# Kernel tuning notes

Hardware: AMD Instinct MI355X
Metric: run time of the kernel (lower is better)

Reference implementation:

```python
import jax, jax.numpy as jnp
import numpy as np

N = 30000      # entities
E = 200000     # KG triples
E_ALL = 400000 # full-graph edges
R = 500        # relations
EH = 300       # e_hidden
RH = 100       # r_hidden
H = 8          # GAT / R2E heads
H_E2R = 2      # E2R heads: int(softmax(head_selector).sum()+1) == 2 always
EPS = 1e-16    # torch_geometric softmax eps


def _seg_softmax(logits, idx, num):
    # logits: [E, heads]; segment-wise stable softmax over edges grouped by idx
    m = jax.ops.segment_max(logits, idx, num_segments=num)
    ex = jnp.exp(logits - m[idx])
    s = jax.ops.segment_sum(ex, idx, num_segments=num)
    return ex / (s[idx] + EPS)


def _gcn(x, ei):
    j, i = ei[0], ei[1]
    deg = jax.ops.segment_sum(jnp.ones(ei.shape[1], x.dtype), i, num_segments=N)
    dis = jnp.where(deg > 0, deg ** -0.5, 0.0)
    norm = dis[j] * dis[i]                                        # [E_all]
    agg = jax.ops.segment_sum(norm[:, None] * x[j], i, num_segments=N)
    return jax.nn.relu(agg)


def _highway(x1, x2, w, b):
    gate = jax.nn.sigmoid(x1 @ w.T + b)
    return gate * x2 + (1.0 - gate) * x1


def setup_inputs() -> dict:
    key = jax.random.key(0)
    ks = jax.random.split(key, 20)
    f = jnp.float32
    inp = {
        'x_e': jax.random.normal(ks[0], (N, EH), f),
        'edge_index': jax.random.randint(ks[1], (2, E), 0, N),
        'rel': jax.random.randint(ks[2], (E,), 0, R),
        'edge_index_all': jax.random.randint(ks[3], (2, E_ALL), 0, N),
        'rel_all': jax.random.randint(ks[4], (E_ALL,), 0, R),
        # Highway layers
        'hw1_w': jax.random.normal(ks[5], (EH, EH), f) / np.sqrt(EH),
        'hw1_b': jnp.zeros((EH,), f),
        'hw2_w': jax.random.normal(ks[6], (EH, EH), f) / np.sqrt(EH),
        'hw2_b': jnp.zeros((EH,), f),
        # E2R (only first H_E2R heads are ever used)
        'e2r_wh': jax.random.normal(ks[7], (RH, EH), f) / np.sqrt(EH),
        'e2r_wt': jax.random.normal(ks[8], (RH, EH), f) / np.sqrt(EH),
        'e2r_ah': jax.random.normal(ks[9], (H_E2R, RH), f) / np.sqrt(RH),
        'e2r_at': jax.random.normal(ks[10], (H_E2R, RH), f) / np.sqrt(RH),
        # R2E
        'r2e_ah': jax.random.normal(ks[11], (H, EH), f) / np.sqrt(EH),
        'r2e_at': jax.random.normal(ks[12], (H, EH), f) / np.sqrt(EH),
        'r2e_ar': jax.random.normal(ks[13], (H, RH), f) / np.sqrt(RH),
        # GAT over e_hidden + 2*r_hidden = 500
        'gat_ai': jax.random.normal(ks[14], (H, EH + 2 * RH), f) / np.sqrt(EH + 2 * RH),
        'gat_aj': jax.random.normal(ks[15], (H, EH + 2 * RH), f) / np.sqrt(EH + 2 * RH),
    }
    return inp


def reference(x_e, edge_index, rel, edge_index_all, rel_all,
              hw1_w, hw1_b, hw2_w, hw2_b,
              e2r_wh, e2r_wt, e2r_ah, e2r_at,
              r2e_ah, r2e_at, r2e_ar, gat_ai, gat_aj):
    lrelu = jax.nn.leaky_relu  # slope 0.01, matches torch default

    # --- two GCN + Highway blocks (dropout = identity at eval) ---
    x = _highway(x_e, _gcn(x_e, edge_index_all), hw1_w, hw1_b)
    x = _highway(x, _gcn(x, edge_index_all), hw2_w, hw2_b)

    h_idx, t_idx = edge_index[0], edge_index[1]

    # --- E2R: entity -> relation (2 heads; spmm sum over heads folded into alpha sum) ---
    xh = x @ e2r_wh.T                        # [N, RH]
    xt = x @ e2r_wt.T                        # [N, RH]
    e1 = (xh @ e2r_ah.T)[h_idx] + (xt @ e2r_at.T)[t_idx]   # [E, H_E2R]
    a1 = _seg_softmax(lrelu(e1), rel, R)
    xr_h = jax.ops.segment_sum(a1.sum(1)[:, None] * xh[h_idx], rel, num_segments=R)
    e2 = (xt @ e2r_ah.T)[h_idx] + (xh @ e2r_at.T)[t_idx]
    a2 = _seg_softmax(lrelu(e2), rel, R)
    xr_t = jax.ops.segment_sum(a2.sum(1)[:, None] * xt[t_idx], rel, num_segments=R)
    x_r = (xr_h + xr_t) / H_E2R / 2.0        # [R, RH]

    # --- R2E: relation -> entity (8 heads) ---
    se_h = x @ r2e_ah.T                      # [N, H]
    se_t = x @ r2e_at.T
    sr = x_r @ r2e_ar.T                      # [R, H]
    a_h = _seg_softmax(lrelu(se_h[h_idx] + sr[rel]), h_idx, N)
    a_t = _seg_softmax(lrelu(se_t[t_idx] + sr[rel]), t_idx, N)
    xr_rel = x_r[rel]                        # [E, RH]
    xe_h = jax.ops.segment_sum(a_h.sum(1)[:, None] * xr_rel, h_idx, num_segments=N) / H
    xe_t = jax.ops.segment_sum(a_t.sum(1)[:, None] * xr_rel, t_idx, num_segments=N) / H
    x2 = jnp.concatenate([x, xe_h, xe_t], axis=1)          # [N, EH+2*RH]

    # --- GAT over full graph (8 heads) ---
    j_a, i_a = edge_index_all[0], edge_index_all[1]
    e_ij = (x2 @ gat_ai.T)[i_a] + (x2 @ gat_aj.T)[j_a]     # [E_all, H]
    al = _seg_softmax(lrelu(e_ij), i_a, N)
    x_gat = jax.ops.segment_sum(al.sum(1)[:, None] * x2[j_a], i_a, num_segments=N) / H

    return jnp.concatenate([x2, x_gat], axis=1)            # [N, 2*(EH+2*RH)]
```

## Files before the change

### kernel.cpp

```cpp
#include <hip/hip_runtime.h>
#include <math.h>

constexpr int N_    = 30000;
constexpr int E_    = 200000;
constexpr int EALL_ = 400000;
constexpr int R_    = 500;
constexpr int EH_   = 300;
constexpr int RH_   = 100;
constexpr int OUTD_ = 1000;
constexpr int LD4   = OUTD_/4;
constexpr int EH4   = EH_/4;
constexpr int RH4   = RH_/4;
constexpr int NC_   = 16;
constexpr int XBS_  = 320;
constexpr int XEBS_ = 200;
constexpr int KP_   = 320;
constexpr int NBR_  = 64;
constexpr int PERB_ = (E_ + NBR_ - 1)/NBR_;
constexpr int SCB_  = 2048;
constexpr int NSB_  = (N_ + SCB_ - 1)/SCB_;
constexpr int SCNP_ = NSB_*SCB_;

typedef __attribute__((ext_vector_type(4))) float f32x4;
typedef __attribute__((ext_vector_type(8))) short s16x8;

__device__ __forceinline__ float lrelu_(float v){ return v > 0.f ? v : 0.01f*v; }
__device__ __forceinline__ float sig_(float z){ return 1.f/(1.f + expf(-z)); }
__device__ __forceinline__ unsigned short f2bf_(float f){
  unsigned int u = __float_as_uint(f);
  unsigned int r = (u + 0x7FFFu + ((u >> 16) & 1u)) >> 16;
  return (unsigned short)r;
}
__device__ __forceinline__ float bf2f_(unsigned short h){
  return __uint_as_float(((unsigned int)h) << 16);
}

__global__ void k_count3(const int* __restrict__ ia,
                         const int* __restrict__ hi, const int* __restrict__ ti,
                         int* cd, int* ch, int* ct){
  int idx = blockIdx.x*blockDim.x + threadIdx.x;
  if (idx < EALL_) { atomicAdd(&cd[ia[idx]], 1); return; }
  idx -= EALL_;
  if (idx < E_) { atomicAdd(&ch[hi[idx]], 1); return; }
  idx -= E_;
  if (idx < E_) { atomicAdd(&ct[ti[idx]], 1); return; }
}

__global__ void k_scanA(const int* __restrict__ c0, const int* __restrict__ c1,
                        const int* __restrict__ c2, int* __restrict__ bsum){
  int arr = blockIdx.x / NSB_, b = blockIdx.x - arr*NSB_;
  const int* c = arr == 0 ? c0 : (arr == 1 ? c1 : c2);
  int t = threadIdx.x;
  const int4* c4 = reinterpret_cast<const int4*>(c + b*SCB_ + t*8);
  int4 u0 = c4[0], u1 = c4[1];
  int acc = u0.x+u0.y+u0.z+u0.w + u1.x+u1.y+u1.z+u1.w;
  __shared__ int red[256];
  red[t] = acc;
  __syncthreads();
  for (int o = 128; o > 0; o >>= 1){
    if (t < o) red[t] += red[t+o];
    __syncthreads();
  }
  if (t == 0) bsum[arr*NSB_ + b] = red[0];
}

__global__ void k_scanB(int* __restrict__ bsum, int* o0, int* o1, int* o2){
  int t = threadIdx.x;
  if (t < 3){
    int run = 0;
    for (int b = 0; b < NSB_; ++b){ int v = bsum[t*NSB_ + b]; bsum[t*NSB_ + b] = run; run += v; }
    int* o = t == 0 ? o0 : (t == 1 ? o1 : o2);
    o[N_] = run;
  }
}

__global__ void k_scanC(const int* __restrict__ c0, const int* __restrict__ c1,
                        const int* __restrict__ c2, const int* __restrict__ bsum,
                        int* o0, int* o1, int* o2, float* __restrict__ dis){
  int arr = blockIdx.x / NSB_, b = blockIdx.x - arr*NSB_;
  const int* c = arr == 0 ? c0 : (arr == 1 ? c1 : c2);
  int* o = arr == 0 ? o0 : (arr == 1 ? o1 : o2);
  int t = threadIdx.x;
  int base = b*SCB_ + t*8;
  const int4* c4 = reinterpret_cast<const int4*>(c + base);
  int4 u0 = c4[0], u1 = c4[1];
  int v[8] = {u0.x,u0.y,u0.z,u0.w,u1.x,u1.y,u1.z,u1.w};
  int tot = v[0]+v[1]+v[2]+v[3]+v[4]+v[5]+v[6]+v[7];
  __shared__ int sc[256];
  sc[t] = tot;
  __syncthreads();
  for (int off = 1; off < 256; off <<= 1){
    int add = (t >= off) ? sc[t-off] : 0;
    __syncthreads();
    sc[t] += add;
    __syncthreads();
  }
  int run = bsum[arr*NSB_ + b] + (t ? sc[t-1] : 0);
  #pragma unroll
  for (int i = 0; i < 8; ++i){
    int idx = base + i;
    o[idx] = run;
    if (arr == 0) dis[idx] = v[i] > 0 ? rsqrtf((float)v[i]) : 0.f;
    run += v[i];
  }
}

__global__ void k_scatter3(const int* __restrict__ ja, const int* __restrict__ ia,
                           const int* __restrict__ rel, const int* __restrict__ hi,
                           const int* __restrict__ ti,
                           const int* od, const int* oh, const int* ot,
                           int* curd, int* curh, int* curt,
                           const float* __restrict__ dis,
                           int* j_dest, float* wj,
                           int* relh, int* relt){
  int idx = blockIdx.x*blockDim.x + threadIdx.x;
  if (idx < EALL_){
    int e = idx, s = ia[e];
    int p = od[s] + atomicAdd(&curd[s], 1);
    int j = ja[e];
    j_dest[p] = j; wj[p] = dis[j]; return;
  }
  idx -= EALL_;
  if (idx < E_){
    int e = idx, s = hi[e];
    int p = oh[s] + atomicAdd(&curh[s], 1);
    relh[p] = rel[e]; return;
  }
  idx -= E_;
  if (idx < E_){
    int e = idx, s = ti[e];
    int p = ot[s] + atomicAdd(&curt[s], 1);
    relt[p] = rel[e]; return;
  }
}

__global__ void k_relhist(const int* __restrict__ rel, int* __restrict__ H){
  __shared__ int h[R_];
  int b = blockIdx.x, tid = threadIdx.x;
  for (int i = tid; i < R_; i += 256) h[i] = 0;
  __syncthreads();
  int s = b*PERB_, e = min(s + PERB_, E_);
  for (int i = s + tid; i < e; i += 256) atomicAdd(&h[rel[i]], 1);
  __syncthreads();
  for (int i = tid; i < R_; i += 256) H[b*R_ + i] = h[i];
}

__global__ void k_relscan(int* __restrict__ H, int* __restrict__ off_rel){
  __shared__ int tot[R_];
  __shared__ int sc[256];
  int tid = threadIdx.x;
  for (int r = tid; r < R_; r += 256){
    int acc = 0;
    for (int b = 0; b < NBR_; ++b){ int v = H[b*R_ + r]; H[b*R_ + r] = acc; acc += v; }
    tot[r] = acc;
  }
  __syncthreads();
  int r0 = tid*2;
  int a0 = (r0 < R_) ? tot[r0] : 0;
  int a1 = (r0+1 < R_) ? tot[r0+1] : 0;
  sc[tid] = a0 + a1;
  __syncthreads();
  for (int off = 1; off < 256; off <<= 1){
    int add = (tid >= off) ? sc[tid-off] : 0;
    __syncthreads();
    sc[tid] += add;
    __syncthreads();
  }
  int run = tid ? sc[tid-1] : 0;
  if (r0 < R_)   off_rel[r0]   = run;
  if (r0+1 < R_) off_rel[r0+1] = run + a0;
  if (tid == 255) off_rel[R_] = sc[255];
  __syncthreads();
  for (int r = tid; r < R_; r += 256){
    int o = off_rel[r];
    for (int b = 0; b < NBR_; ++b) H[b*R_ + r] += o;
  }
}

__global__ void k_relscatter(const int* __restrict__ rel, const int* __restrict__ hi,
                             const int* __restrict__ ti, const int* __restrict__ H,
                             int* __restrict__ hr, int* __restrict__ tr){
  __shared__ int cur[R_];
  int b = blockIdx.x, tid = threadIdx.x;
  for (int i = tid; i < R_; i += 256) cur[i] = H[b*R_ + i];
  __syncthreads();
  int s = b*PERB_, e = min(s + PERB_, E_);
  for (int i = s + tid; i < e; i += 256){
    int r = rel[i];
    int p = atomicAdd(&cur[r], 1);
    hr[p] = hi[i]; tr[p] = ti[i];
  }
}

__global__ void k_pack_x(const float4* __restrict__ X, int ldx4,
                         unsigned short* __restrict__ xb){
  int idx = blockIdx.x*blockDim.x + threadIdx.x;
  if (idx >= N_*80) return;
  int n = idx / 80, c = idx - n*80;
  ushort4 o = make_ushort4(0,0,0,0);
  if (c < EH4){
    float4 v = X[(size_t)n*ldx4 + c];
    o.x = f2bf_(v.x); o.y = f2bf_(v.y); o.z = f2bf_(v.z); o.w = f2bf_(v.w);
  }
  *reinterpret_cast<ushort4*>(&xb[(size_t)n*XBS_ + c*4]) = o;
}

__global__ void k_pack_weights(const float* __restrict__ w1, const float* __restrict__ w2,
                               const float* __restrict__ wh, const float* __restrict__ wt,
                               unsigned short* w1b, unsigned short* w2b,
                               unsigned short* wcb){
  int idx = blockIdx.x*blockDim.x + threadIdx.x;
  if (idx < EH_*KP_){
    int n = idx/KP_, k = idx - n*KP_;
    w1b[idx] = (k < EH_) ? f2bf_(w1[(size_t)n*EH_ + k]) : (unsigned short)0;
    return;
  }
  idx -= EH_*KP_;
  if (idx < EH_*KP_){
    int n = idx/KP_, k = idx - n*KP_;
    w2b[idx] = (k < EH_) ? f2bf_(w2[(size_t)n*EH_ + k]) : (unsigned short)0;
    return;
  }
  idx -= EH_*KP_;
  if (idx < 200*KP_){
    int n = idx/KP_, k = idx - n*KP_;
    wcb[idx] = (k < EH_) ? f2bf_((n < 100) ? wh[(size_t)n*EH_ + k] : wt[(size_t)(n-100)*EH_ + k])
                         : (unsigned short)0;
  }
}

__global__ __launch_bounds__(256) void k_gemm_mfma(
    const unsigned short* __restrict__ Ab,
    const unsigned short* __restrict__ Wb,
    float* __restrict__ C, int ldc, int M, int Nn){
  constexpr int WS = 328;
  constexpr int AS = 40;
  __shared__ unsigned short Ws[64*WS];
  __shared__ unsigned short As[128*AS];
  int tid = threadIdx.x;
  int lane = tid & 63, wave = tid >> 6;
  int wm = wave & 1, wn = wave >> 1;
  int m0 = blockIdx.x*128, n0 = blockIdx.y*64;

  for (int c = tid; c < 64*(KP_/8); c += 256){
    int n = c / (KP_/8), k8 = (c % (KP_/8))*8;
    s16x8 v = {0,0,0,0,0,0,0,0};
    if (n0 + n < Nn)
      v = *reinterpret_cast<const s16x8*>(&Wb[(size_t)(n0+n)*KP_ + k8]);
    *reinterpret_cast<s16x8*>(&Ws[n*WS + k8]) = v;
  }

  f32x4 acc[4][2] = {};
  int kf = (lane >> 4)*8;
  int rA = lane & 15;
  for (int k0 = 0; k0 < KP_; k0 += 32){
    __syncthreads();
    for (int c = tid; c < 128*4; c += 256){
      int r = c >> 2, k8 = (c & 3)*8;
      s16x8 v = {0,0,0,0,0,0,0,0};
      if (m0 + r < M)
        v = *reinterpret_cast<const s16x8*>(&Ab[(size_t)(m0+r)*XBS_ + k0 + k8]);
      *reinterpret_cast<s16x8*>(&As[r*AS + k8]) = v;
    }
    __syncthreads();
    s16x8 afr[4], bfr[2];
    #pragma unroll
    for (int mf = 0; mf < 4; ++mf)
      afr[mf] = *reinterpret_cast<const s16x8*>(&As[(wm*64 + mf*16 + rA)*AS + kf]);
    #pragma unroll
    for (int nf = 0; nf < 2; ++nf)
      bfr[nf] = *reinterpret_cast<const s16x8*>(&Ws[(wn*32 + nf*16 + rA)*WS + k0 + kf]);
    #pragma unroll
    for (int mf = 0; mf < 4; ++mf)
      #pragma unroll
      for (int nf = 0; nf < 2; ++nf)
        acc[mf][nf] = __builtin_amdgcn_mfma_f32_16x16x32_bf16(afr[mf], bfr[nf], acc[mf][nf], 0, 0, 0);
  }
  int col0 = n0 + wn*32 + (lane & 15);
  int rbase = m0 + wm*64 + (lane >> 4)*4;
  #pragma unroll
  for (int mf = 0; mf < 4; ++mf){
    #pragma unroll
    for (int nf = 0; nf < 2; ++nf){
      int col = col0 + nf*16;
      if (col < Nn){
        #pragma unroll
        for (int r = 0; r < 4; ++r){
          int row = rbase + mf*16 + r;
          if (row < M) C[(size_t)row*ldc + col] = acc[mf][nf][r];
        }
      }
    }
  }
}

__global__ void k_gcn5(const int* __restrict__ off, const int* __restrict__ jd,
                       const float* __restrict__ wj, const float* __restrict__ dis,
                       const unsigned short* __restrict__ xsrc,
                       const float4* __restrict__ Xold, int ldo4,
                       const float4* __restrict__ G, const float* __restrict__ b,
                       float4* __restrict__ Xn, unsigned short* __restrict__ xdst){
  __shared__ int js[64];
  __shared__ float ws[64];
  int n = blockIdx.x, lane = threadIdx.x;
  int s = off[n], t = off[n+1];
  bool two = lane < (EH4 - 64);
  float4 a0 = make_float4(0.f,0.f,0.f,0.f);
  float4 a1 = make_float4(0.f,0.f,0.f,0.f);
  for (int base = s; base < t; base += 64){
    int m = min(64, t - base);
    __syncthreads();
    if (lane < m){ js[lane] = jd[base+lane]; ws[lane] = wj[base+lane]; }
    __syncthreads();
    int q = 0;
    for (; q + 3 < m; q += 4){
      size_t r0 = (size_t)js[q]*XBS_,   r1 = (size_t)js[q+1]*XBS_;
      size_t r2 = (size_t)js[q+2]*XBS_, r3 = (size_t)js[q+3]*XBS_;
      float w0 = ws[q], w1 = ws[q+1], w2 = ws[q+2], w3 = ws[q+3];
      ushort4 u0 = *reinterpret_cast<const ushort4*>(&xsrc[r0 + lane*4]);
      ushort4 u1 = *reinterpret_cast<const ushort4*>(&xsrc[r1 + lane*4]);
      ushort4 u2 = *reinterpret_cast<const ushort4*>(&xsrc[r2 + lane*4]);
      ushort4 u3 = *reinterpret_cast<const ushort4*>(&xsrc[r3 + lane*4]);
      a0.x += w0*bf2f_(u0.x)+w1*bf2f_(u1.x)+w2*bf2f_(u2.x)+w3*bf2f_(u3.x);
      a0.y += w0*bf2f_(u0.y)+w1*bf2f_(u1.y)+w2*bf2f_(u2.y)+w3*bf2f_(u3.y);
      a0.z += w0*bf2f_(u0.z)+w1*bf2f_(u1.z)+w2*bf2f_(u2.z)+w3*bf2f_(u3.z);
      a0.w += w0*bf2f_(u0.w)+w1*bf2f_(u1.w)+w2*bf2f_(u2.w)+w3*bf2f_(u3.w);
      if (two){
        ushort4 v0 = *reinterpret_cast<const ushort4*>(&xsrc[r0 + 256 + lane*4]);
        ushort4 v1 = *reinterpret_cast<const ushort4*>(&xsrc[r1 + 256 + lane*4]);
        ushort4 v2 = *reinterpret_cast<const ushort4*>(&xsrc[r2 + 256 + lane*4]);
        ushort4 v3 = *reinterpret_cast<const ushort4*>(&xsrc[r3 + 256 + lane*4]);
        a1.x += w0*bf2f_(v0.x)+w1*bf2f_(v1.x)+w2*bf2f_(v2.x)+w3*bf2f_(v3.x);
        a1.y += w0*bf2f_(v0.y)+w1*bf2f_(v1.y)+w2*bf2f_(v2.y)+w3*bf2f_(v3.y);
        a1.z += w0*bf2f_(v0.z)+w1*bf2f_(v1.z)+w2*bf2f_(v2.z)+w3*bf2f_(v3.z);
        a1.w += w0*bf2f_(v0.w)+w1*bf2f_(v1.w)+w2*bf2f_(v2.w)+w3*bf2f_(v3.w);
      }
    }
    for (; q < m; ++q){
      size_t r0 = (size_t)js[q]*XBS_;
      float w0 = ws[q];
      ushort4 u0 = *reinterpret_cast<const ushort4*>(&xsrc[r0 + lane*4]);
      a0.x += w0*bf2f_(u0.x); a0.y += w0*bf2f_(u0.y);
      a0.z += w0*bf2f_(u0.z); a0.w += w0*bf2f_(u0.w);
      if (two){
        ushort4 v0 = *reinterpret_cast<const ushort4*>(&xsrc[r0 + 256 + lane*4]);
        a1.x += w0*bf2f_(v0.x); a1.y += w0*bf2f_(v0.y);
        a1.z += w0*bf2f_(v0.z); a1.w += w0*bf2f_(v0.w);
      }
    }
  }
  float dn = dis[n];
  {
    int c = lane;
    float4 yv;
    yv.x = fmaxf(dn*a0.x, 0.f); yv.y = fmaxf(dn*a0.y, 0.f);
    yv.z = fmaxf(dn*a0.z, 0.f); yv.w = fmaxf(dn*a0.w, 0.f);
    float4 g4 = G[(size_t)n*EH4 + c];
    float4 b4 = reinterpret_cast<const float4*>(b)[c];
    float4 xo = Xold[(size_t)n*ldo4 + c];
    float gx; float4 r;
    gx = sig_(g4.x + b4.x); r.x = gx*yv.x + (1.f-gx)*xo.x;
    gx = sig_(g4.y + b4.y); r.y = gx*yv.y + (1.f-gx)*xo.y;
    gx = sig_(g4.z + b4.z); r.z = gx*yv.z + (1.f-gx)*xo.z;
    gx = sig_(g4.w + b4.w); r.w = gx*yv.w + (1.f-gx)*xo.w;
    Xn[(size_t)n*LD4 + c] = r;
    ushort4 o;
    o.x = f2bf_(r.x); o.y = f2bf_(r.y); o.z = f2bf_(r.z); o.w = f2bf_(r.w);
    *reinterpret_cast<ushort4*>(&xdst[(size_t)n*XBS_ + c*4]) = o;
  }
  if (two){
    int c = 64 + lane;
    float4 yv;
    yv.x = fmaxf(dn*a1.x, 0.f); yv.y = fmaxf(dn*a1.y, 0.f);
    yv.z = fmaxf(dn*a1.z, 0.f); yv.w = fmaxf(dn*a1.w, 0.f);
    float4 g4 = G[(size_t)n*EH4 + c];
    float4 b4 = reinterpret_cast<const float4*>(b)[c];
    float4 xo = Xold[(size_t)n*ldo4 + c];
    float gx; float4 r;
    gx = sig_(g4.x + b4.x); r.x = gx*yv.x + (1.f-gx)*xo.x;
    gx = sig_(g4.y + b4.y); r.y = gx*yv.y + (1.f-gx)*xo.y;
    gx = sig_(g4.z + b4.z); r.z = gx*yv.z + (1.f-gx)*xo.z;
    gx = sig_(g4.w + b4.w); r.w = gx*yv.w + (1.f-gx)*xo.w;
    Xn[(size_t)n*LD4 + c] = r;
    ushort4 o;
    o.x = f2bf_(r.x); o.y = f2bf_(r.y); o.z = f2bf_(r.z); o.w = f2bf_(r.w);
    *reinterpret_cast<ushort4*>(&xdst[(size_t)n*XBS_ + c*4]) = o;
  } else if (lane < 16){
    ushort4 z = make_ushort4(0,0,0,0);
    *reinterpret_cast<ushort4*>(&xdst[(size_t)n*XBS_ + (64+lane)*4]) = z;
  }
}

__global__ void k_pproj(const float* __restrict__ xhxt,
                        const float* __restrict__ ah, const float* __restrict__ at,
                        float4* __restrict__ pht){
  int n = blockIdx.x*blockDim.x + threadIdx.x;
  if (n >= N_) return;
  float a0=0,a1=0,b0=0,b1=0,c0=0,c1=0,d0=0,d1=0;
  const float* xh = xhxt + (size_t)n*200;
  const float* xt = xh + 100;
  for (int f = 0; f < RH_; ++f) {
    float vh = xh[f], vt = xt[f];
    float w0 = ah[f], w1 = ah[RH_+f], u0 = at[f], u1 = at[RH_+f];
    a0 += vh*w0; a1 += vh*w1;
    b0 += vt*u0; b1 += vt*u1;
    c0 += vt*w0; c1 += vt*w1;
    d0 += vh*u0; d1 += vh*u1;
  }
  pht[(size_t)n*2]     = make_float4(a0, a1, c0, c1);
  pht[(size_t)n*2 + 1] = make_float4(b0, b1, d0, d1);
}

__global__ void k_fold_rel2(const int* __restrict__ off,
                            const int* __restrict__ hr, const int* __restrict__ tr,
                            const float4* __restrict__ pht,
                            float* __restrict__ s1p, float* __restrict__ s2p){
  __shared__ float4 redm[4];
  __shared__ float4 reds[4];
  int r = blockIdx.x;
  int tid = threadIdx.x, lane = tid & 63, w = tid >> 6;
  int s = off[r], e = off[r+1];
  float4 mx = make_float4(-1e30f,-1e30f,-1e30f,-1e30f);
  for (int p = s + tid; p < e; p += 256){
    float4 ph = pht[(size_t)hr[p]*2];
    float4 pt = pht[(size_t)tr[p]*2 + 1];
    mx.x = fmaxf(mx.x, lrelu_(ph.x + pt.x));
    mx.y = fmaxf(mx.y, lrelu_(ph.y + pt.y));
    mx.z = fmaxf(mx.z, lrelu_(ph.z + pt.z));
    mx.w = fmaxf(mx.w, lrelu_(ph.w + pt.w));
  }
  #pragma unroll
  for (int o = 1; o < 64; o <<= 1){
    mx.x = fmaxf(mx.x, __shfl_xor(mx.x, o));
    mx.y = fmaxf(mx.y, __shfl_xor(mx.y, o));
    mx.z = fmaxf(mx.z, __shfl_xor(mx.z, o));
    mx.w = fmaxf(mx.w, __shfl_xor(mx.w, o));
  }
  if (lane == 0) redm[w] = mx;
  __syncthreads();
  float4 m;
  m.x = fmaxf(fmaxf(redm[0].x, redm[1].x), fmaxf(redm[2].x, redm[3].x));
  m.y = fmaxf(fmaxf(redm[0].y, redm[1].y), fmaxf(redm[2].y, redm[3].y));
  m.z = fmaxf(fmaxf(redm[0].z, redm[1].z), fmaxf(redm[2].z, redm[3].z));
  m.w = fmaxf(fmaxf(redm[0].w, redm[1].w), fmaxf(redm[2].w, redm[3].w));
  float4 sm = make_float4(0.f,0.f,0.f,0.f);
  for (int p = s + tid; p < e; p += 256){
    float4 ph = pht[(size_t)hr[p]*2];
    float4 pt = pht[(size_t)tr[p]*2 + 1];
    sm.x += expf(lrelu_(ph.x + pt.x) - m.x);
    sm.y += expf(lrelu_(ph.y + pt.y) - m.y);
    sm.z += expf(lrelu_(ph.z + pt.z) - m.z);
    sm.w += expf(lrelu_(ph.w + pt.w) - m.w);
  }
  #pragma unroll
  for (int o = 1; o < 64; o <<= 1){
    sm.x += __shfl_xor(sm.x, o);
    sm.y += __shfl_xor(sm.y, o);
    sm.z += __shfl_xor(sm.z, o);
    sm.w += __shfl_xor(sm.w, o);
  }
  if (lane == 0) reds[w] = sm;
  __syncthreads();
  float4 sv;
  sv.x = reds[0].x + reds[1].x + reds[2].x + reds[3].x;
  sv.y = reds[0].y + reds[1].y + reds[2].y + reds[3].y;
  sv.z = reds[0].z + reds[1].z + reds[2].z + reds[3].z;
  sv.w = reds[0].w + reds[1].w + reds[2].w + reds[3].w;
  float4 inv;
  inv.x = 1.f/(sv.x + 1e-16f); inv.y = 1.f/(sv.y + 1e-16f);
  inv.z = 1.f/(sv.z + 1e-16f); inv.w = 1.f/(sv.w + 1e-16f);
  for (int p = s + tid; p < e; p += 256){
    float4 ph = pht[(size_t)hr[p]*2];
    float4 pt = pht[(size_t)tr[p]*2 + 1];
    s1p[p] = expf(lrelu_(ph.x + pt.x) - m.x)*inv.x + expf(lrelu_(ph.y + pt.y) - m.y)*inv.y;
    s2p[p] = expf(lrelu_(ph.z + pt.z) - m.z)*inv.z + expf(lrelu_(ph.w + pt.w) - m.w)*inv.w;
  }
}

__global__ void k_fold_ht2(const int* __restrict__ offh, const int* __restrict__ offt,
                           const int* __restrict__ relh, const int* __restrict__ relt,
                           const float* __restrict__ st16, const float* __restrict__ sr8,
                           float* __restrict__ shp, float* __restrict__ stp){
  int w = threadIdx.x >> 6, lane = threadIdx.x & 63;
  int n = blockIdx.x*2 + (w >> 1);
  if (n >= N_) return;
  int side = w & 1;
  const int* off = side ? offt : offh;
  const int* rl  = side ? relt : relh;
  float* op = side ? stp : shp;
  int k = lane & 7, g = lane >> 3;
  float cst = st16[(size_t)n*16 + side*8 + k];
  int s = off[n], e = off[n+1];
  float m = -1e30f;
  for (int p = s + g; p < e; p += 8)
    m = fmaxf(m, lrelu_(cst + sr8[(size_t)rl[p]*8 + k]));
  #pragma unroll
  for (int o = 8; o < 64; o <<= 1) m = fmaxf(m, __shfl_xor(m, o));
  float sum = 0.f;
  for (int p = s + g; p < e; p += 8)
    sum += expf(lrelu_(cst + sr8[(size_t)rl[p]*8 + k]) - m);
  #pragma unroll
  for (int o = 8; o < 64; o <<= 1) sum += __shfl_xor(sum, o);
  float inv = 1.f / (sum + 1e-16f);
  for (int p = s + g; p < e; p += 8){
    float t = expf(lrelu_(cst + sr8[(size_t)rl[p]*8 + k]) - m) * inv;
    #pragma unroll
    for (int o = 1; o < 8; o <<= 1) t += __shfl_xor(t, o);
    if (k == 0) op[p] = t;
  }
}

__global__ void k_fold_gat2(const int* __restrict__ off, const int* __restrict__ jd,
                            const float* __restrict__ gg16, float* __restrict__ agp){
  int w = threadIdx.x >> 6, lane = threadIdx.x & 63;
  int n = blockIdx.x*4 + w;
  if (n >= N_) return;
  int k = lane & 7, g = lane >> 3;
  float cst = gg16[(size_t)n*16 + k];
  int s = off[n], e = off[n+1];
  float m = -1e30f;
  for (int p = s + g; p < e; p += 8)
    m = fmaxf(m, lrelu_(cst + gg16[(size_t)jd[p]*16 + 8 + k]));
  #pragma unroll
  for (int o = 8; o < 64; o <<= 1) m = fmaxf(m, __shfl_xor(m, o));
  float sum = 0.f;
  for (int p = s + g; p < e; p += 8)
    sum += expf(lrelu_(cst + gg16[(size_t)jd[p]*16 + 8 + k]) - m);
  #pragma unroll
  for (int o = 8; o < 64; o <<= 1) sum += __shfl_xor(sum, o);
  float inv = 1.f / (sum + 1e-16f);
  for (int p = s + g; p < e; p += 8){
    float t = expf(lrelu_(cst + gg16[(size_t)jd[p]*16 + 8 + k]) - m) * inv;
    #pragma unroll
    for (int o = 1; o < 8; o <<= 1) t += __shfl_xor(t, o);
    if (k == 0) agp[p] = t;
  }
}

__global__ void k_e2r_agg3(const int* __restrict__ off,
                           const int* __restrict__ hr, const int* __restrict__ tr,
                           const float* __restrict__ s1p, const float* __restrict__ s2p,
                           const float4* __restrict__ xhxt4, float4* __restrict__ xr_part){
  int r = blockIdx.x, c = blockIdx.y;
  int lane = threadIdx.x;
  int side = lane >> 5, fl = lane & 31;
  int s = off[r], e = off[r+1];
  int len = e - s;
  int per = (len + NC_ - 1)/NC_;
  int cs = s + c*per, ce = min(cs + per, e);
  float4 acc = make_float4(0.f,0.f,0.f,0.f);
  if (fl < RH4){
    const int* idx = side ? tr : hr;
    const float* wv = side ? s2p : s1p;
    int fofs = side ? 25 + fl : fl;
    int p = cs;
    for (; p + 1 < ce; p += 2){
      float a0 = wv[p], a1 = wv[p+1];
      float4 v0 = xhxt4[(size_t)idx[p]*50 + fofs];
      float4 v1 = xhxt4[(size_t)idx[p+1]*50 + fofs];
      acc.x += a0*v0.x + a1*v1.x; acc.y += a0*v0.y + a1*v1.y;
      acc.z += a0*v0.z + a1*v1.z; acc.w += a0*v0.w + a1*v1.w;
    }
    if (p < ce){
      float a0 = wv[p];
      float4 v0 = xhxt4[(size_t)idx[p]*50 + fofs];
      acc.x += a0*v0.x; acc.y += a0*v0.y; acc.z += a0*v0.z; acc.w += a0*v0.w;
    }
  }
  float4 oth;
  oth.x = __shfl_xor(acc.x, 32); oth.y = __shfl_xor(acc.y, 32);
  oth.z = __shfl_xor(acc.z, 32); oth.w = __shfl_xor(acc.w, 32);
  if (side == 0 && fl < RH4){
    float4 o = make_float4(acc.x+oth.x, acc.y+oth.y, acc.z+oth.z, acc.w+oth.w);
    xr_part[((size_t)c*R_ + r)*RH4 + fl] = o;
  }
}

__global__ void k_e2r_red2(const float4* __restrict__ xr_part, float4* __restrict__ xr4,
                           const float* __restrict__ ar, float* __restrict__ sr8){
  __shared__ float row[RH_];
  int r = blockIdx.x, lane = threadIdx.x;
  if (lane < RH4){
    float4 a = make_float4(0.f,0.f,0.f,0.f);
    #pragma unroll
    for (int c = 0; c < NC_; ++c){
      float4 v = xr_part[((size_t)c*R_ + r)*RH4 + lane];
      a.x += v.x; a.y += v.y; a.z += v.z; a.w += v.w;
    }
    a.x *= 0.25f; a.y *= 0.25f; a.z *= 0.25f; a.w *= 0.25f;
    xr4[(size_t)r*RH4 + lane] = a;
    row[lane*4]   = a.x; row[lane*4+1] = a.y;
    row[lane*4+2] = a.z; row[lane*4+3] = a.w;
  }
  __syncthreads();
  int h = lane & 7, gk = lane >> 3;
  float acc = 0.f;
  for (int k = gk; k < RH_; k += 8) acc += row[k]*ar[(size_t)h*RH_ + k];
  #pragma unroll
  for (int o = 8; o < 64; o <<= 1) acc += __shfl_xor(acc, o);
  if (lane < 8) sr8[(size_t)r*8 + lane] = acc;
}

__global__ void k_dots16b(const unsigned short* __restrict__ X, int ldx, int K, int colofs, int Kw,
                          const float* __restrict__ wA, const float* __restrict__ wB,
                          float* __restrict__ out16, int M, int accum){
  __shared__ float xs[16][65];
  __shared__ float ws[16][65];
  int tid = threadIdx.x;
  int tx = tid & 15, ty = tid >> 4;
  int r0 = blockIdx.x*16;
  int lr = tid >> 4;
  int lc = (tid & 15)*4;
  float acc = 0.f;
  for (int c0 = 0; c0 < K; c0 += 64){
    int cl = min(64, K - c0);
    float4 xv = make_float4(0.f,0.f,0.f,0.f);
    if (r0 + lr < M && lc < cl){
      ushort4 u = *reinterpret_cast<const ushort4*>(&X[(size_t)(r0+lr)*ldx + c0 + lc]);
      xv.x = bf2f_(u.x); xv.y = bf2f_(u.y); xv.z = bf2f_(u.z); xv.w = bf2f_(u.w);
    }
    float4 wv = make_float4(0.f,0.f,0.f,0.f);
    if (lc < cl){
      const float* wsrc = (lr < 8) ? &wA[(size_t)lr*Kw + colofs + c0 + lc]
                                   : &wB[(size_t)(lr-8)*Kw + colofs + c0 + lc];
      wv = *reinterpret_cast<const float4*>(wsrc);
    }
    xs[lr][lc] = xv.x; xs[lr][lc+1] = xv.y; xs[lr][lc+2] = xv.z; xs[lr][lc+3] = xv.w;
    ws[lr][lc] = wv.x; ws[lr][lc+1] = wv.y; ws[lr][lc+2] = wv.z; ws[lr][lc+3] = wv.w;
    __syncthreads();
    #pragma unroll
    for (int k = 0; k < 64; ++k) acc += xs[ty][k]*ws[tx][k];
    __syncthreads();
  }
  if (r0 + ty < M){
    size_t o = (size_t)(r0+ty)*16 + tx;
    out16[o] = accum ? out16[o] + acc : acc;
  }
}

__global__ void k_r2e_agg2b(const int* __restrict__ offh, const int* __restrict__ offt,
                            const int* __restrict__ relh, const int* __restrict__ relt,
                            const float* __restrict__ shp, const float* __restrict__ stp,
                            const float4* __restrict__ xr4, float4* __restrict__ out,
                            unsigned short* __restrict__ xeb){
  int n = blockIdx.x;
  int side = threadIdx.x >> 6, lane = threadIdx.x & 63;
  const int* off = side ? offt : offh;
  const int* rr  = side ? relt : relh;
  const float* sp = side ? stp : shp;
  int s = off[n], e = off[n+1];
  if (lane >= RH4) return;
  float4 acc = make_float4(0.f,0.f,0.f,0.f);
  int p = s;
  for (; p + 1 < e; p += 2){
    float a0 = sp[p], a1 = sp[p+1];
    float4 v0 = xr4[(size_t)rr[p]*RH4 + lane];
    float4 v1 = xr4[(size_t)rr[p+1]*RH4 + lane];
    acc.x += a0*v0.x + a1*v1.x; acc.y += a0*v0.y + a1*v1.y;
    acc.z += a0*v0.z + a1*v1.z; acc.w += a0*v0.w + a1*v1.w;
  }
  if (p < e){
    float a0 = sp[p];
    float4 v0 = xr4[(size_t)rr[p]*RH4 + lane];
    acc.x += a0*v0.x; acc.y += a0*v0.y; acc.z += a0*v0.z; acc.w += a0*v0.w;
  }
  float4 o = make_float4(acc.x*0.125f, acc.y*0.125f, acc.z*0.125f, acc.w*0.125f);
  out[(size_t)n*LD4 + (side ? 100 : 75) + lane] = o;
  ushort4 ob;
  ob.x = f2bf_(o.x); ob.y = f2bf_(o.y); ob.z = f2bf_(o.z); ob.w = f2bf_(o.w);
  *reinterpret_cast<ushort4*>(&xeb[(size_t)n*XEBS_ + (side ? 100 : 0) + lane*4]) = ob;
}

__global__ void k_gat_agg4(const int* __restrict__ off, const int* __restrict__ jd,
                           const float* __restrict__ agp,
                           const unsigned short* __restrict__ xb,
                           const unsigned short* __restrict__ xeb,
                           float4* __restrict__ out){
  __shared__ int js[128];
  __shared__ float as_[128];
  int n = blockIdx.x, tid = threadIdx.x;
  int s = off[n], t = off[n+1];
  const unsigned short* tbl;
  size_t stride; int cofs;
  if (tid < 75){ tbl = xb;  stride = XBS_;  cofs = tid*4; }
  else         { tbl = xeb; stride = XEBS_; cofs = (tid-75)*4; }
  float4 acc = make_float4(0.f,0.f,0.f,0.f);
  for (int base = s; base < t; base += 128){
    int m = min(128, t - base);
    __syncthreads();
    if (tid < m){ js[tid] = jd[base+tid]; as_[tid] = agp[base+tid]; }
    __syncthreads();
    if (tid < 125){
      int q = 0;
      for (; q + 3 < m; q += 4){
        float a0 = as_[q], a1 = as_[q+1], a2 = as_[q+2], a3 = as_[q+3];
        ushort4 u0 = *reinterpret_cast<const ushort4*>(&tbl[(size_t)js[q]*stride + cofs]);
        ushort4 u1 = *reinterpret_cast<const ushort4*>(&tbl[(size_t)js[q+1]*stride + cofs]);
        ushort4 u2 = *reinterpret_cast<const ushort4*>(&tbl[(size_t)js[q+2]*stride + cofs]);
        ushort4 u3 = *reinterpret_cast<const ushort4*>(&tbl[(size_t)js[q+3]*stride + cofs]);
        acc.x += a0*bf2f_(u0.x)+a1*bf2f_(u1.x)+a2*bf2f_(u2.x)+a3*bf2f_(u3.x);
        acc.y += a0*bf2f_(u0.y)+a1*bf2f_(u1.y)+a2*bf2f_(u2.y)+a3*bf2f_(u3.y);
        acc.z += a0*bf2f_(u0.z)+a1*bf2f_(u1.z)+a2*bf2f_(u2.z)+a3*bf2f_(u3.z);
        acc.w += a0*bf2f_(u0.w)+a1*bf2f_(u1.w)+a2*bf2f_(u2.w)+a3*bf2f_(u3.w);
      }
      for (; q < m; ++q){
        float a0 = as_[q];
        ushort4 u0 = *reinterpret_cast<const ushort4*>(&tbl[(size_t)js[q]*stride + cofs]);
        acc.x += a0*bf2f_(u0.x); acc.y += a0*bf2f_(u0.y);
        acc.z += a0*bf2f_(u0.z); acc.w += a0*bf2f_(u0.w);
      }
    }
  }
  if (tid < 125){
    float4 r = make_float4(acc.x*0.125f, acc.y*0.125f, acc.z*0.125f, acc.w*0.125f);
    out[(size_t)n*LD4 + 125 + tid] = r;
  }
}

static inline void gemm_mfma(const unsigned short* Ab, const unsigned short* Wb,
                             float* C, int ldc, int M, int Nn, hipStream_t st){
  dim3 g((M + 127)/128, (Nn + 63)/64);
  k_gemm_mfma<<<g, 256, 0, st>>>(Ab, Wb, C, ldc, M, Nn);
}

extern "C" void kernel_launch(void* const* d_in, const int* in_sizes, int n_in,
                              void* d_out, int out_size, void* d_ws, size_t ws_size,
                              hipStream_t stream) {
  const float* x_e   = (const float*)d_in[0];
  const int*   ei    = (const int*)d_in[1];
  const int*   rel   = (const int*)d_in[2];
  const int*   eia   = (const int*)d_in[3];
  const float* hw1_w = (const float*)d_in[5];
  const float* hw1_b = (const float*)d_in[6];
  const float* hw2_w = (const float*)d_in[7];
  const float* hw2_b = (const float*)d_in[8];
  const float* e2r_wh= (const float*)d_in[9];
  const float* e2r_wt= (const float*)d_in[10];
  const float* e2r_ah= (const float*)d_in[11];
  const float* e2r_at= (const float*)d_in[12];
  const float* r2e_ah= (const float*)d_in[13];
  const float* r2e_at= (const float*)d_in[14];
  const float* r2e_ar= (const float*)d_in[15];
  const float* gat_ai= (const float*)d_in[16];
  const float* gat_aj= (const float*)d_in[17];
  float* out = (float*)d_out;

  const int* hi = ei;
  const int* ti = ei + E_;
  const int* ja = eia;
  const int* ia = eia + EALL_;

  char* base = (char*)d_ws;
  size_t off = 0;
  auto alloc = [&](size_t bytes)->void*{
    void* p = base + off;
    off = (off + bytes + 255) & ~(size_t)255;
    return p;
  };

  size_t z0 = off;
  int* cnt_dest = (int*)alloc(SCNP_*4);
  int* cnt_h    = (int*)alloc(SCNP_*4);
  int* cnt_t    = (int*)alloc(SCNP_*4);
  int* cur_dest = (int*)alloc(N_*4);
  int* cur_h    = (int*)alloc(N_*4);
  int* cur_t    = (int*)alloc(N_*4);
  size_t z1 = off;

  int* off_dest = (int*)alloc(SCNP_*4);
  int* off_h    = (int*)alloc(SCNP_*4);
  int* off_t    = (int*)alloc(SCNP_*4);
  int* off_rel  = (int*)alloc((R_+1)*4);
  int* bsum     = (int*)alloc(3*NSB_*4);
  int* Hrel     = (int*)alloc((size_t)NBR_*R_*4);
  int* j_dest   = (int*)alloc((size_t)EALL_*4);
  int* hr       = (int*)alloc((size_t)E_*4);
  int* tr       = (int*)alloc((size_t)E_*4);
  int* relh     = (int*)alloc((size_t)E_*4);
  int* relt     = (int*)alloc((size_t)E_*4);

  float* dis   = (float*)alloc(SCNP_*4);
  float* wj    = (float*)alloc((size_t)EALL_*4);
  float* g     = (float*)alloc((size_t)N_*EH_*4);
  float* xhxt  = (float*)alloc((size_t)N_*200*4);
  float* pht   = (float*)alloc((size_t)N_*8*4);
  float* s1p   = (float*)alloc((size_t)E_*4);
  float* s2p   = (float*)alloc((size_t)E_*4);
  float* xr    = (float*)alloc((size_t)R_*RH_*4);
  float* xr_part=(float*)alloc((size_t)NC_*R_*RH_*4);
  float* st16  = (float*)alloc((size_t)N_*16*4);
  float* sr8   = (float*)alloc((size_t)R_*8*4);
  float* shp   = (float*)alloc((size_t)E_*4);
  float* stp   = (float*)alloc((size_t)E_*4);
  float* gg16  = (float*)alloc((size_t)N_*16*4);
  float* agp   = (float*)alloc((size_t)EALL_*4);
  unsigned short* xbA = (unsigned short*)alloc((size_t)N_*XBS_*2);
  unsigned short* xbB = (unsigned short*)alloc((size_t)N_*XBS_*2);
  unsigned short* xeb = (unsigned short*)alloc((size_t)N_*XEBS_*2);
  unsigned short* w1b = (unsigned short*)alloc((size_t)EH_*KP_*2);
  unsigned short* w2b = (unsigned short*)alloc((size_t)EH_*KP_*2);
  unsigned short* wcb = (unsigned short*)alloc((size_t)200*KP_*2);

  hipMemsetAsync(base + z0, 0, z1 - z0, stream);

  const int TB = 256;
  const int TOT = EALL_ + 2*E_;
  int gTOT  = (TOT + TB - 1)/TB;
  int gN    = (N_ + TB - 1)/TB;
  int gPKX  = (N_*80 + TB - 1)/TB;
  const int WTOT = 2*EH_*KP_ + 200*KP_;

  k_pack_weights<<<(WTOT + TB - 1)/TB, TB, 0, stream>>>(hw1_w, hw2_w, e2r_wh, e2r_wt,
                                                        w1b, w2b, wcb);

  k_relhist<<<NBR_, 256, 0, stream>>>(rel, Hrel);
  k_relscan<<<1, 256, 0, stream>>>(Hrel, off_rel);
  k_relscatter<<<NBR_, 256, 0, stream>>>(rel, hi, ti, Hrel, hr, tr);

  k_count3<<<gTOT, TB, 0, stream>>>(ia, hi, ti, cnt_dest, cnt_h, cnt_t);
  k_scanA<<<3*NSB_, 256, 0, stream>>>(cnt_dest, cnt_h, cnt_t, bsum);
  k_scanB<<<1, 64, 0, stream>>>(bsum, off_dest, off_h, off_t);
  k_scanC<<<3*NSB_, 256, 0, stream>>>(cnt_dest, cnt_h, cnt_t, bsum,
                                      off_dest, off_h, off_t, dis);
  k_scatter3<<<gTOT, TB, 0, stream>>>(ja, ia, rel, hi, ti,
                                      off_dest, off_h, off_t,
                                      cur_dest, cur_h, cur_t,
                                      dis, j_dest, wj, relh, relt);

  k_pack_x<<<gPKX, TB, 0, stream>>>((const float4*)x_e, EH4, xbA);
  gemm_mfma(xbA, w1b, g, EH_, N_, EH_, stream);
  k_gcn5<<<N_, 64, 0, stream>>>(off_dest, j_dest, wj, dis, xbA,
                                (const float4*)x_e, EH4, (const float4*)g, hw1_b,
                                (float4*)out, xbB);
  gemm_mfma(xbB, w2b, g, EH_, N_, EH_, stream);
  k_gcn5<<<N_, 64, 0, stream>>>(off_dest, j_dest, wj, dis, xbB,
                                (const float4*)out, LD4, (const float4*)g, hw2_b,
                                (float4*)out, xbA);

  gemm_mfma(xbA, wcb, xhxt, 200, N_, 200, stream);
  k_pproj<<<gN, TB, 0, stream>>>(xhxt, e2r_ah, e2r_at, (float4*)pht);
  k_fold_rel2<<<R_, 256, 0, stream>>>(off_rel, hr, tr, (const float4*)pht, s1p, s2p);
  k_e2r_agg3<<<dim3(R_, NC_), 64, 0, stream>>>(off_rel, hr, tr, s1p, s2p,
                                               (const float4*)xhxt, (float4*)xr_part);
  k_e2r_red2<<<R_, 64, 0, stream>>>((const float4*)xr_part, (float4*)xr, r2e_ar, sr8);

  k_dots16b<<<(N_+15)/16, 256, 0, stream>>>(xbA, XBS_, EH_, 0, EH_, r2e_ah, r2e_at, st16, N_, 0);
  k_fold_ht2<<<(N_+1)/2, 256, 0, stream>>>(off_h, off_t, relh, relt, st16, sr8, shp, stp);
  k_r2e_agg2b<<<N_, 128, 0, stream>>>(off_h, off_t, relh, relt, shp, stp,
                                      (const float4*)xr, (float4*)out, xeb);

  k_dots16b<<<(N_+15)/16, 256, 0, stream>>>(xbA, XBS_, EH_, 0, 500, gat_ai, gat_aj, gg16, N_, 0);
  k_dots16b<<<(N_+15)/16, 256, 0, stream>>>(xeb, XEBS_, 200, EH_, 500, gat_ai, gat_aj, gg16, N_, 1);
  k_fold_gat2<<<(N_+3)/4, 256, 0, stream>>>(off_dest, j_dest, gg16, agp);
  k_gat_agg4<<<N_, 128, 0, stream>>>(off_dest, j_dest, agp, xbA, xeb, (float4*)out);
}
```

Measured before the change: 624.9 us.

## Fuse softmax folds into aggregation kernels and merge graph-build launches

Folds the segment-softmax passes for R2E and GAT into their aggregation kernels, which removes the per-edge attention buffers (shp, stp, agp) and their separate launches. It also merges the preprocessing kernels (weight and x packing, relation histogram with degree counting, relation scan with block scan, and the two scatters) into fewer launches. The two GAT dot kernels become one that reads both bf16 tables. The gcn kernel now takes the highway residual from the bf16 copy instead of the fp32 one, which cuts bandwidth but lowers the precision of that term. The fused GAT kernel recomputes exp for 8 heads per edge inside each block.

Result: faster. 578.7 us (-7.4%).

```diff
diff --git a/kernel.cpp b/kernel.cpp
--- a/kernel.cpp
+++ b/kernel.cpp
@@ -35,10 +35,58 @@
   return __uint_as_float(((unsigned int)h) << 16);
 }
 
-__global__ void k_count3(const int* __restrict__ ia,
+__global__ void k_pack_all(const float* __restrict__ w1, const float* __restrict__ w2,
+                           const float* __restrict__ wh, const float* __restrict__ wt,
+                           const float4* __restrict__ Xe,
+                           unsigned short* w1b, unsigned short* w2b,
+                           unsigned short* wcb, unsigned short* xb){
+  int idx = blockIdx.x*blockDim.x + threadIdx.x;
+  if (idx < EH_*KP_){
+    int n = idx/KP_, k = idx - n*KP_;
+    w1b[idx] = (k < EH_) ? f2bf_(w1[(size_t)n*EH_ + k]) : (unsigned short)0;
+    return;
+  }
+  idx -= EH_*KP_;
+  if (idx < EH_*KP_){
+    int n = idx/KP_, k = idx - n*KP_;
+    w2b[idx] = (k < EH_) ? f2bf_(w2[(size_t)n*EH_ + k]) : (unsigned short)0;
+    return;
+  }
+  idx -= EH_*KP_;
+  if (idx < 200*KP_){
+    int n = idx/KP_, k = idx - n*KP_;
+    wcb[idx] = (k < EH_) ? f2bf_((n < 100) ? wh[(size_t)n*EH_ + k] : wt[(size_t)(n-100)*EH_ + k])
+                         : (unsigned short)0;
+    return;
+  }
+  idx -= 200*KP_;
+  if (idx < N_*80){
+    int n = idx/80, c = idx - n*80;
+    ushort4 o = make_ushort4(0,0,0,0);
+    if (c < EH4){
+      float4 v = Xe[(size_t)n*EH4 + c];
+      o.x = f2bf_(v.x); o.y = f2bf_(v.y); o.z = f2bf_(v.z); o.w = f2bf_(v.w);
+    }
+    *reinterpret_cast<ushort4*>(&xb[(size_t)n*XBS_ + c*4]) = o;
+  }
+}
+
+__global__ void k_build1(const int* __restrict__ rel, const int* __restrict__ ia,
                          const int* __restrict__ hi, const int* __restrict__ ti,
-                         int* cd, int* ch, int* ct){
-  int idx = blockIdx.x*blockDim.x + threadIdx.x;
+                         int* __restrict__ H, int* cd, int* ch, int* ct){
+  __shared__ int h[R_];
+  int tid = threadIdx.x;
+  if ((int)blockIdx.x < NBR_){
+    int b = blockIdx.x;
+    for (int i = tid; i < R_; i += 256) h[i] = 0;
+    __syncthreads();
+    int s = b*PERB_, e = min(s + PERB_, E_);
+    for (int i = s + tid; i < e; i += 256) atomicAdd(&h[rel[i]], 1);
+    __syncthreads();
+    for (int i = tid; i < R_; i += 256) H[b*R_ + i] = h[i];
+    return;
+  }
+  int idx = (blockIdx.x - NBR_)*256 + tid;
   if (idx < EALL_) { atomicAdd(&cd[ia[idx]], 1); return; }
   idx -= EALL_;
   if (idx < E_) { atomicAdd(&ch[hi[idx]], 1); return; }
@@ -64,13 +112,45 @@
   if (t == 0) bsum[arr*NSB_ + b] = red[0];
 }
 
-__global__ void k_scanB(int* __restrict__ bsum, int* o0, int* o1, int* o2){
-  int t = threadIdx.x;
-  if (t < 3){
-    int run = 0;
-    for (int b = 0; b < NSB_; ++b){ int v = bsum[t*NSB_ + b]; bsum[t*NSB_ + b] = run; run += v; }
-    int* o = t == 0 ? o0 : (t == 1 ? o1 : o2);
-    o[N_] = run;
+__global__ void k_mid(int* __restrict__ H, int* __restrict__ off_rel,
+                      int* __restrict__ bsum, int* o0, int* o1, int* o2){
+  __shared__ int tot[R_];
+  __shared__ int sc[256];
+  int tid = threadIdx.x;
+  if (blockIdx.x == 1){
+    if (tid < 3){
+      int run = 0;
+      for (int b = 0; b < NSB_; ++b){ int v = bsum[tid*NSB_ + b]; bsum[tid*NSB_ + b] = run; run += v; }
+      int* o = tid == 0 ? o0 : (tid == 1 ? o1 : o2);
+      o[N_] = run;
+    }
+    return;
+  }
+  for (int r = tid; r < R_; r += 256){
+    int acc = 0;
+    for (int b = 0; b < NBR_; ++b){ int v = H[b*R_ + r]; H[b*R_ + r] = acc; acc += v; }
+    tot[r] = acc;
+  }
+  __syncthreads();
+  int r0 = tid*2;
+  int a0 = (r0 < R_) ? tot[r0] : 0;
+  int a1 = (r0+1 < R_) ? tot[r0+1] : 0;
+  sc[tid] = a0 + a1;
+  __syncthreads();
+  for (int off = 1; off < 256; off <<= 1){
+    int add = (tid >= off) ? sc[tid-off] : 0;
+    __syncthreads();
+    sc[tid] += add;
+    __syncthreads();
+  }
+  int run = tid ? sc[tid-1] : 0;
+  if (r0 < R_)   off_rel[r0]   = run;
+  if (r0+1 < R_) off_rel[r0+1] = run + a0;
+  if (tid == 255) off_rel[R_] = sc[255];
+  __syncthreads();
+  for (int r = tid; r < R_; r += 256){
+    int o = off_rel[r];
+    for (int b = 0; b < NBR_; ++b) H[b*R_ + r] += o;
   }
 }
 
@@ -105,15 +185,29 @@
   }
 }
 
-__global__ void k_scatter3(const int* __restrict__ ja, const int* __restrict__ ia,
-                           const int* __restrict__ rel, const int* __restrict__ hi,
-                           const int* __restrict__ ti,
-                           const int* od, const int* oh, const int* ot,
-                           int* curd, int* curh, int* curt,
-                           const float* __restrict__ dis,
-                           int* j_dest, float* wj,
-                           int* relh, int* relt){
-  int idx = blockIdx.x*blockDim.x + threadIdx.x;
+__global__ void k_build2(const int* __restrict__ rel, const int* __restrict__ hi,
+                         const int* __restrict__ ti, const int* __restrict__ H,
+                         int* __restrict__ hr, int* __restrict__ tr,
+                         const int* __restrict__ ja, const int* __restrict__ ia,
+                         const int* od, const int* oh, const int* ot,
+                         int* curd, int* curh, int* curt,
+                         const float* __restrict__ dis,
+                         int* j_dest, float* wj, int* relh, int* relt){
+  __shared__ int cur[R_];
+  int tid = threadIdx.x;
+  if ((int)blockIdx.x < NBR_){
+    int b = blockIdx.x;
+    for (int i = tid; i < R_; i += 256) cur[i] = H[b*R_ + i];
+    __syncthreads();
+    int s = b*PERB_, e = min(s + PERB_, E_);
+    for (int i = s + tid; i < e; i += 256){
+      int r = rel[i];
+      int p = atomicAdd(&cur[r], 1);
+      hr[p] = hi[i]; tr[p] = ti[i];
+    }
+    return;
+  }
+  int idx = (blockIdx.x - NBR_)*256 + tid;
   if (idx < EALL_){
     int e = idx, s = ia[e];
     int p = od[s] + atomicAdd(&curd[s], 1);
@@ -131,101 +225,6 @@
     int e = idx, s = ti[e];
     int p = ot[s] + atomicAdd(&curt[s], 1);
     relt[p] = rel[e]; return;
-  }
-}
-
-__global__ void k_relhist(const int* __restrict__ rel, int* __restrict__ H){
-  __shared__ int h[R_];
-  int b = blockIdx.x, tid = threadIdx.x;
-  for (int i = tid; i < R_; i += 256) h[i] = 0;
-  __syncthreads();
-  int s = b*PERB_, e = min(s + PERB_, E_);
-  for (int i = s + tid; i < e; i += 256) atomicAdd(&h[rel[i]], 1);
-  __syncthreads();
-  for (int i = tid; i < R_; i += 256) H[b*R_ + i] = h[i];
-}
-
-__global__ void k_relscan(int* __restrict__ H, int* __restrict__ off_rel){
-  __shared__ int tot[R_];
-  __shared__ int sc[256];
-  int tid = threadIdx.x;
-  for (int r = tid; r < R_; r += 256){
-    int acc = 0;
-    for (int b = 0; b < NBR_; ++b){ int v = H[b*R_ + r]; H[b*R_ + r] = acc; acc += v; }
-    tot[r] = acc;
-  }
-  __syncthreads();
-  int r0 = tid*2;
-  int a0 = (r0 < R_) ? tot[r0] : 0;
-  int a1 = (r0+1 < R_) ? tot[r0+1] : 0;
-  sc[tid] = a0 + a1;
-  __syncthreads();
-  for (int off = 1; off < 256; off <<= 1){
-    int add = (tid >= off) ? sc[tid-off] : 0;
-    __syncthreads();
-    sc[tid] += add;
-    __syncthreads();
-  }
-  int run = tid ? sc[tid-1] : 0;
-  if (r0 < R_)   off_rel[r0]   = run;
-  if (r0+1 < R_) off_rel[r0+1] = run + a0;
-  if (tid == 255) off_rel[R_] = sc[255];
-  __syncthreads();
-  for (int r = tid; r < R_; r += 256){
-    int o = off_rel[r];
-    for (int b = 0; b < NBR_; ++b) H[b*R_ + r] += o;
-  }
-}
-
-__global__ void k_relscatter(const int* __restrict__ rel, const int* __restrict__ hi,
-                             const int* __restrict__ ti, const int* __restrict__ H,
-                             int* __restrict__ hr, int* __restrict__ tr){
-  __shared__ int cur[R_];
-  int b = blockIdx.x, tid = threadIdx.x;
-  for (int i = tid; i < R_; i += 256) cur[i] = H[b*R_ + i];
-  __syncthreads();
-  int s = b*PERB_, e = min(s + PERB_, E_);
-  for (int i = s + tid; i < e; i += 256){
-    int r = rel[i];
-    int p = atomicAdd(&cur[r], 1);
-    hr[p] = hi[i]; tr[p] = ti[i];
-  }
-}
-
-__global__ void k_pack_x(const float4* __restrict__ X, int ldx4,
-                         unsigned short* __restrict__ xb){
-  int idx = blockIdx.x*blockDim.x + threadIdx.x;
-  if (idx >= N_*80) return;
-  int n = idx / 80, c = idx - n*80;
-  ushort4 o = make_ushort4(0,0,0,0);
-  if (c < EH4){
-    float4 v = X[(size_t)n*ldx4 + c];
-    o.x = f2bf_(v.x); o.y = f2bf_(v.y); o.z = f2bf_(v.z); o.w = f2bf_(v.w);
-  }
-  *reinterpret_cast<ushort4*>(&xb[(size_t)n*XBS_ + c*4]) = o;
-}
-
-__global__ void k_pack_weights(const float* __restrict__ w1, const float* __restrict__ w2,
-                               const float* __restrict__ wh, const float* __restrict__ wt,
-                               unsigned short* w1b, unsigned short* w2b,
-                               unsigned short* wcb){
-  int idx = blockIdx.x*blockDim.x + threadIdx.x;
-  if (idx < EH_*KP_){
-    int n = idx/KP_, k = idx - n*KP_;
-    w1b[idx] = (k < EH_) ? f2bf_(w1[(size_t)n*EH_ + k]) : (unsigned short)0;
-    return;
-  }
-  idx -= EH_*KP_;
-  if (idx < EH_*KP_){
-    int n = idx/KP_, k = idx - n*KP_;
-    w2b[idx] = (k < EH_) ? f2bf_(w2[(size_t)n*EH_ + k]) : (unsigned short)0;
-    return;
-  }
-  idx -= EH_*KP_;
-  if (idx < 200*KP_){
-    int n = idx/KP_, k = idx - n*KP_;
-    wcb[idx] = (k < EH_) ? f2bf_((n < 100) ? wh[(size_t)n*EH_ + k] : wt[(size_t)(n-100)*EH_ + k])
-                         : (unsigned short)0;
   }
 }
 
@@ -297,7 +296,6 @@
 __global__ void k_gcn5(const int* __restrict__ off, const int* __restrict__ jd,
                        const float* __restrict__ wj, const float* __restrict__ dis,
                        const unsigned short* __restrict__ xsrc,
-                       const float4* __restrict__ Xold, int ldo4,
                        const float4* __restrict__ G, const float* __restrict__ b,
                        float4* __restrict__ Xn, unsigned short* __restrict__ xdst){
   __shared__ int js[64];
@@ -357,7 +355,8 @@
     yv.z = fmaxf(dn*a0.z, 0.f); yv.w = fmaxf(dn*a0.w, 0.f);
     float4 g4 = G[(size_t)n*EH4 + c];
     float4 b4 = reinterpret_cast<const float4*>(b)[c];
-    float4 xo = Xold[(size_t)n*ldo4 + c];
+    ushort4 uo = *reinterpret_cast<const ushort4*>(&xsrc[(size_t)n*XBS_ + c*4]);
+    float4 xo = make_float4(bf2f_(uo.x), bf2f_(uo.y), bf2f_(uo.z), bf2f_(uo.w));
     float gx; float4 r;
     gx = sig_(g4.x + b4.x); r.x = gx*yv.x + (1.f-gx)*xo.x;
     gx = sig_(g4.y + b4.y); r.y = gx*yv.y + (1.f-gx)*xo.y;
@@ -375,7 +374,8 @@
     yv.z = fmaxf(dn*a1.z, 0.f); yv.w = fmaxf(dn*a1.w, 0.f);
     float4 g4 = G[(size_t)n*EH4 + c];
     float4 b4 = reinterpret_cast<const float4*>(b)[c];
-    float4 xo = Xold[(size_t)n*ldo4 + c];
+    ushort4 uo = *reinterpret_cast<const ushort4*>(&xsrc[(size_t)n*XBS_ + c*4]);
+    float4 xo = make_float4(bf2f_(uo.x), bf2f_(uo.y), bf2f_(uo.z), bf2f_(uo.w));
     float gx; float4 r;
     gx = sig_(g4.x + b4.x); r.x = gx*yv.x + (1.f-gx)*xo.x;
     gx = sig_(g4.y + b4.y); r.y = gx*yv.y + (1.f-gx)*xo.y;
@@ -474,66 +474,6 @@
     float4 pt = pht[(size_t)tr[p]*2 + 1];
     s1p[p] = expf(lrelu_(ph.x + pt.x) - m.x)*inv.x + expf(lrelu_(ph.y + pt.y) - m.y)*inv.y;
     s2p[p] = expf(lrelu_(ph.z + pt.z) - m.z)*inv.z + expf(lrelu_(ph.w + pt.w) - m.w)*inv.w;
-  }
-}
-
-__global__ void k_fold_ht2(const int* __restrict__ offh, const int* __restrict__ offt,
-                           const int* __restrict__ relh, const int* __restrict__ relt,
-                           const float* __restrict__ st16, const float* __restrict__ sr8,
-                           float* __restrict__ shp, float* __restrict__ stp){
-  int w = threadIdx.x >> 6, lane = threadIdx.x & 63;
-  int n = blockIdx.x*2 + (w >> 1);
-  if (n >= N_) return;
-  int side = w & 1;
-  const int* off = side ? offt : offh;
-  const int* rl  = side ? relt : relh;
-  float* op = side ? stp : shp;
-  int k = lane & 7, g = lane >> 3;
-  float cst = st16[(size_t)n*16 + side*8 + k];
-  int s = off[n], e = off[n+1];
-  float m = -1e30f;
-  for (int p = s + g; p < e; p += 8)
-    m = fmaxf(m, lrelu_(cst + sr8[(size_t)rl[p]*8 + k]));
-  #pragma unroll
-  for (int o = 8; o < 64; o <<= 1) m = fmaxf(m, __shfl_xor(m, o));
-  float sum = 0.f;
-  for (int p = s + g; p < e; p += 8)
-    sum += expf(lrelu_(cst + sr8[(size_t)rl[p]*8 + k]) - m);
-  #pragma unroll
-  for (int o = 8; o < 64; o <<= 1) sum += __shfl_xor(sum, o);
-  float inv = 1.f / (sum + 1e-16f);
-  for (int p = s + g; p < e; p += 8){
-    float t = expf(lrelu_(cst + sr8[(size_t)rl[p]*8 + k]) - m) * inv;
-    #pragma unroll
-    for (int o = 1; o < 8; o <<= 1) t += __shfl_xor(t, o);
-    if (k == 0) op[p] = t;
-  }
-}
-
-__global__ void k_fold_gat2(const int* __restrict__ off, const int* __restrict__ jd,
-                            const float* __restrict__ gg16, float* __restrict__ agp){
-  int w = threadIdx.x >> 6, lane = threadIdx.x & 63;
-  int n = blockIdx.x*4 + w;
-  if (n >= N_) return;
-  int k = lane & 7, g = lane >> 3;
-  float cst = gg16[(size_t)n*16 + k];
-  int s = off[n], e = off[n+1];
-  float m = -1e30f;
-  for (int p = s + g; p < e; p += 8)
-    m = fmaxf(m, lrelu_(cst + gg16[(size_t)jd[p]*16 + 8 + k]));
-  #pragma unroll
-  for (int o = 8; o < 64; o <<= 1) m = fmaxf(m, __shfl_xor(m, o));
-  float sum = 0.f;
-  for (int p = s + g; p < e; p += 8)
-    sum += expf(lrelu_(cst + gg16[(size_t)jd[p]*16 + 8 + k]) - m);
-  #pragma unroll
-  for (int o = 8; o < 64; o <<= 1) sum += __shfl_xor(sum, o);
-  float inv = 1.f / (sum + 1e-16f);
-  for (int p = s + g; p < e; p += 8){
-    float t = expf(lrelu_(cst + gg16[(size_t)jd[p]*16 + 8 + k]) - m) * inv;
-    #pragma unroll
-    for (int o = 1; o < 8; o <<= 1) t += __shfl_xor(t, o);
-    if (k == 0) agp[p] = t;
   }
 }
 
@@ -601,9 +541,9 @@
   if (lane < 8) sr8[(size_t)r*8 + lane] = acc;
 }
 
-__global__ void k_dots16b(const unsigned short* __restrict__ X, int ldx, int K, int colofs, int Kw,
+__global__ void k_dots16b(const unsigned short* __restrict__ X, int ldx, int K, int Kw,
                           const float* __restrict__ wA, const float* __restrict__ wB,
-                          float* __restrict__ out16, int M, int accum){
+                          float* __restrict__ out16, int M){
   __shared__ float xs[16][65];
   __shared__ float ws[16][65];
   int tid = threadIdx.x;
@@ -621,8 +561,8 @@
     }
     float4 wv = make_float4(0.f,0.f,0.f,0.f);
     if (lc < cl){
-      const float* wsrc = (lr < 8) ? &wA[(size_t)lr*Kw + colofs + c0 + lc]
-                                   : &wB[(size_t)(lr-8)*Kw + colofs + c0 + lc];
+      const float* wsrc = (lr < 8) ? &wA[(size_t)lr*Kw + c0 + lc]
+                                   : &wB[(size_t)(lr-8)*Kw + c0 + lc];
       wv = *reinterpret_cast<const float4*>(wsrc);
     }
     xs[lr][lc] = xv.x; xs[lr][lc+1] = xv.y; xs[lr][lc+2] = xv.z; xs[lr][lc+3] = xv.w;
@@ -632,67 +572,178 @@
     for (int k = 0; k < 64; ++k) acc += xs[ty][k]*ws[tx][k];
     __syncthreads();
   }
-  if (r0 + ty < M){
-    size_t o = (size_t)(r0+ty)*16 + tx;
-    out16[o] = accum ? out16[o] + acc : acc;
-  }
-}
-
-__global__ void k_r2e_agg2b(const int* __restrict__ offh, const int* __restrict__ offt,
+  if (r0 + ty < M) out16[(size_t)(r0+ty)*16 + tx] = acc;
+}
+
+__global__ void k_dots16g(const unsigned short* __restrict__ xb,
+                          const unsigned short* __restrict__ xeb,
+                          const float* __restrict__ wA, const float* __restrict__ wB,
+                          float* __restrict__ out16, int M){
+  __shared__ float xs[16][65];
+  __shared__ float ws[16][65];
+  int tid = threadIdx.x;
+  int tx = tid & 15, ty = tid >> 4;
+  int r0 = blockIdx.x*16;
+  int lr = tid >> 4;
+  int lc = (tid & 15)*4;
+  float acc = 0.f;
+  for (int c0 = 0; c0 < 500; c0 += 64){
+    int cl = min(64, 500 - c0);
+    int col = c0 + lc;
+    float4 xv = make_float4(0.f,0.f,0.f,0.f);
+    if (r0 + lr < M && lc < cl){
+      ushort4 u = (col < 300)
+        ? *reinterpret_cast<const ushort4*>(&xb[(size_t)(r0+lr)*XBS_ + col])
+        : *reinterpret_cast<const ushort4*>(&xeb[(size_t)(r0+lr)*XEBS_ + col - 300]);
+      xv.x = bf2f_(u.x); xv.y = bf2f_(u.y); xv.z = bf2f_(u.z); xv.w = bf2f_(u.w);
+    }
+    float4 wv = make_float4(0.f,0.f,0.f,0.f);
+    if (lc < cl){
+      const float* wsrc = (lr < 8) ? &wA[(size_t)lr*500 + col]
+                                   : &wB[(size_t)(lr-8)*500 + col];
+      wv = *reinterpret_cast<const float4*>(wsrc);
+    }
+    xs[lr][lc] = xv.x; xs[lr][lc+1] = xv.y; xs[lr][lc+2] = xv.z; xs[lr][lc+3] = xv.w;
+    ws[lr][lc] = wv.x; ws[lr][lc+1] = wv.y; ws[lr][lc+2] = wv.z; ws[lr][lc+3] = wv.w;
+    __syncthreads();
+    #pragma unroll
+    for (int k = 0; k < 64; ++k) acc += xs[ty][k]*ws[tx][k];
+    __syncthreads();
+  }
+  if (r0 + ty < M) out16[(size_t)(r0+ty)*16 + tx] = acc;
+}
+
+__global__ void k_r2e_fused(const int* __restrict__ offh, const int* __restrict__ offt,
                             const int* __restrict__ relh, const int* __restrict__ relt,
-                            const float* __restrict__ shp, const float* __restrict__ stp,
+                            const float* __restrict__ st16, const float* __restrict__ sr8,
                             const float4* __restrict__ xr4, float4* __restrict__ out,
                             unsigned short* __restrict__ xeb){
   int n = blockIdx.x;
   int side = threadIdx.x >> 6, lane = threadIdx.x & 63;
   const int* off = side ? offt : offh;
-  const int* rr  = side ? relt : relh;
-  const float* sp = side ? stp : shp;
+  const int* rl  = side ? relt : relh;
   int s = off[n], e = off[n+1];
-  if (lane >= RH4) return;
+  int k = lane & 7, g = lane >> 3;
+  float cst = st16[(size_t)n*16 + side*8 + k];
+  float m = -1e30f;
+  for (int p = s + g; p < e; p += 8)
+    m = fmaxf(m, lrelu_(cst + sr8[(size_t)rl[p]*8 + k]));
+  #pragma unroll
+  for (int o = 8; o < 64; o <<= 1) m = fmaxf(m, __shfl_xor(m, o));
+  float sum = 0.f;
+  for (int p = s + g; p < e; p += 8)
+    sum += expf(lrelu_(cst + sr8[(size_t)rl[p]*8 + k]) - m);
+  #pragma unroll
+  for (int o = 8; o < 64; o <<= 1) sum += __shfl_xor(sum, o);
+  float inv = 1.f / (sum + 1e-16f);
+  float mks[8], invs[8], csts[8];
+  int gb = lane & 56;
+  #pragma unroll
+  for (int kk = 0; kk < 8; ++kk){
+    mks[kk]  = __shfl(m,   gb + kk);
+    invs[kk] = __shfl(inv, gb + kk);
+    csts[kk] = __shfl(cst, gb + kk);
+  }
   float4 acc = make_float4(0.f,0.f,0.f,0.f);
-  int p = s;
-  for (; p + 1 < e; p += 2){
-    float a0 = sp[p], a1 = sp[p+1];
-    float4 v0 = xr4[(size_t)rr[p]*RH4 + lane];
-    float4 v1 = xr4[(size_t)rr[p+1]*RH4 + lane];
-    acc.x += a0*v0.x + a1*v1.x; acc.y += a0*v0.y + a1*v1.y;
-    acc.z += a0*v0.z + a1*v1.z; acc.w += a0*v0.w + a1*v1.w;
-  }
-  if (p < e){
-    float a0 = sp[p];
-    float4 v0 = xr4[(size_t)rr[p]*RH4 + lane];
-    acc.x += a0*v0.x; acc.y += a0*v0.y; acc.z += a0*v0.z; acc.w += a0*v0.w;
-  }
-  float4 o = make_float4(acc.x*0.125f, acc.y*0.125f, acc.z*0.125f, acc.w*0.125f);
-  out[(size_t)n*LD4 + (side ? 100 : 75) + lane] = o;
-  ushort4 ob;
-  ob.x = f2bf_(o.x); ob.y = f2bf_(o.y); ob.z = f2bf_(o.z); ob.w = f2bf_(o.w);
-  *reinterpret_cast<ushort4*>(&xeb[(size_t)n*XEBS_ + (side ? 100 : 0) + lane*4]) = ob;
-}
-
-__global__ void k_gat_agg4(const int* __restrict__ off, const int* __restrict__ jd,
-                           const float* __restrict__ agp,
-                           const unsigned short* __restrict__ xb,
-                           const unsigned short* __restrict__ xeb,
-                           float4* __restrict__ out){
+  for (int base = s; base < e; base += 64){
+    int mm = min(64, e - base);
+    int rlv = 0; float alpha = 0.f;
+    if (lane < mm){
+      rlv = rl[base + lane];
+      const float4* sr4 = reinterpret_cast<const float4*>(&sr8[(size_t)rlv*8]);
+      float4 s0 = sr4[0], s1 = sr4[1];
+      float sv[8] = {s0.x,s0.y,s0.z,s0.w,s1.x,s1.y,s1.z,s1.w};
+      #pragma unroll
+      for (int kk = 0; kk < 8; ++kk)
+        alpha += expf(lrelu_(csts[kk] + sv[kk]) - mks[kk]) * invs[kk];
+    }
+    for (int q = 0; q < mm; ++q){
+      float a = __shfl(alpha, q);
+      int rr = __shfl(rlv, q);
+      if (lane < RH4){
+        float4 v = xr4[(size_t)rr*RH4 + lane];
+        acc.x += a*v.x; acc.y += a*v.y; acc.z += a*v.z; acc.w += a*v.w;
+      }
+    }
+  }
+  if (lane < RH4){
+    float4 o = make_float4(acc.x*0.125f, acc.y*0.125f, acc.z*0.125f, acc.w*0.125f);
+    out[(size_t)n*LD4 + (side ? 100 : 75) + lane] = o;
+    ushort4 ob;
+    ob.x = f2bf_(o.x); ob.y = f2bf_(o.y); ob.z = f2bf_(o.z); ob.w = f2bf_(o.w);
+    *reinterpret_cast<ushort4*>(&xeb[(size_t)n*XEBS_ + (side ? 100 : 0) + lane*4]) = ob;
+  }
+}
+
+__global__ void k_gat_fused(const int* __restrict__ off, const int* __restrict__ jd,
+                            const float* __restrict__ gg16,
+                            const unsigned short* __restrict__ xb,
+                            const unsigned short* __restrict__ xeb,
+                            float4* __restrict__ out){
   __shared__ int js[128];
   __shared__ float as_[128];
+  __shared__ float wred[2][8];
+  __shared__ float mkS[8], invS[8], cstS[8];
   int n = blockIdx.x, tid = threadIdx.x;
+  int wv = tid >> 6, lane = tid & 63;
   int s = off[n], t = off[n+1];
+  int k = tid & 7, g = tid >> 3;
+  float cst = gg16[(size_t)n*16 + k];
+  float m = -1e30f;
+  for (int p = s + g; p < t; p += 16){
+    int j = jd[p];
+    m = fmaxf(m, lrelu_(cst + gg16[(size_t)j*16 + 8 + k]));
+  }
+  #pragma unroll
+  for (int o = 8; o < 64; o <<= 1) m = fmaxf(m, __shfl_xor(m, o));
+  if (lane < 8) wred[wv][lane] = m;
+  __syncthreads();
+  if (tid < 8) mkS[tid] = fmaxf(wred[0][tid], wred[1][tid]);
+  __syncthreads();
+  float mk = mkS[k];
+  float sum = 0.f;
+  for (int p = s + g; p < t; p += 16){
+    int j = jd[p];
+    sum += expf(lrelu_(cst + gg16[(size_t)j*16 + 8 + k]) - mk);
+  }
+  #pragma unroll
+  for (int o = 8; o < 64; o <<= 1) sum += __shfl_xor(sum, o);
+  if (lane < 8) wred[wv][lane] = sum;
+  __syncthreads();
+  if (tid < 8){
+    invS[tid] = 1.f / (wred[0][tid] + wred[1][tid] + 1e-16f);
+    cstS[tid] = gg16[(size_t)n*16 + tid];
+  }
+  __syncthreads();
   const unsigned short* tbl;
   size_t stride; int cofs;
   if (tid < 75){ tbl = xb;  stride = XBS_;  cofs = tid*4; }
   else         { tbl = xeb; stride = XEBS_; cofs = (tid-75)*4; }
   float4 acc = make_float4(0.f,0.f,0.f,0.f);
   for (int base = s; base < t; base += 128){
-    int m = min(128, t - base);
-    __syncthreads();
-    if (tid < m){ js[tid] = jd[base+tid]; as_[tid] = agp[base+tid]; }
+    int mm = min(128, t - base);
+    __syncthreads();
+    if (tid < mm) js[tid] = jd[base+tid];
+    __syncthreads();
+    if (tid < mm){
+      int j = js[tid];
+      const float4* gj = reinterpret_cast<const float4*>(&gg16[(size_t)j*16 + 8]);
+      float4 l0 = gj[0], l1 = gj[1];
+      float a = 0.f;
+      a += expf(lrelu_(cstS[0] + l0.x) - mkS[0]) * invS[0];
+      a += expf(lrelu_(cstS[1] + l0.y) - mkS[1]) * invS[1];
+      a += expf(lrelu_(cstS[2] + l0.z) - mkS[2]) * invS[2];
+      a += expf(lrelu_(cstS[3] + l0.w) - mkS[3]) * invS[3];
+      a += expf(lrelu_(cstS[4] + l1.x) - mkS[4]) * invS[4];
+      a += expf(lrelu_(cstS[5] + l1.y) - mkS[5]) * invS[5];
+      a += expf(lrelu_(cstS[6] + l1.z) - mkS[6]) * invS[6];
+      a += expf(lrelu_(cstS[7] + l1.w) - mkS[7]) * invS[7];
+      as_[tid] = a;
+    }
     __syncthreads();
     if (tid < 125){
       int q = 0;
-      for (; q + 3 < m; q += 4){
+      for (; q + 3 < mm; q += 4){
         float a0 = as_[q], a1 = as_[q+1], a2 = as_[q+2], a3 = as_[q+3];
         ushort4 u0 = *reinterpret_cast<const ushort4*>(&tbl[(size_t)js[q]*stride + cofs]);
         ushort4 u1 = *reinterpret_cast<const ushort4*>(&tbl[(size_t)js[q+1]*stride + cofs]);
@@ -703,7 +754,7 @@
         acc.z += a0*bf2f_(u0.z)+a1*bf2f_(u1.z)+a2*bf2f_(u2.z)+a3*bf2f_(u3.z);
         acc.w += a0*bf2f_(u0.w)+a1*bf2f_(u1.w)+a2*bf2f_(u2.w)+a3*bf2f_(u3.w);
       }
-      for (; q < m; ++q){
+      for (; q < mm; ++q){
         float a0 = as_[q];
         ushort4 u0 = *reinterpret_cast<const ushort4*>(&tbl[(size_t)js[q]*stride + cofs]);
         acc.x += a0*bf2f_(u0.x); acc.y += a0*bf2f_(u0.y);
@@ -790,10 +841,7 @@
   float* xr_part=(float*)alloc((size_t)NC_*R_*RH_*4);
   float* st16  = (float*)alloc((size_t)N_*16*4);
   float* sr8   = (float*)alloc((size_t)R_*8*4);
-  float* shp   = (float*)alloc((size_t)E_*4);
-  float* stp   = (float*)alloc((size_t)E_*4);
   float* gg16  = (float*)alloc((size_t)N_*16*4);
-  float* agp   = (float*)alloc((size_t)EALL_*4);
   unsigned short* xbA = (unsigned short*)alloc((size_t)N_*XBS_*2);
   unsigned short* xbB = (unsigned short*)alloc((size_t)N_*XBS_*2);
   unsigned short* xeb = (unsigned short*)alloc((size_t)N_*XEBS_*2);
@@ -807,35 +855,28 @@
   const int TOT = EALL_ + 2*E_;
   int gTOT  = (TOT + TB - 1)/TB;
   int gN    = (N_ + TB - 1)/TB;
-  int gPKX  = (N_*80 + TB - 1)/TB;
-  const int WTOT = 2*EH_*KP_ + 200*KP_;
-
-  k_pack_weights<<<(WTOT + TB - 1)/TB, TB, 0, stream>>>(hw1_w, hw2_w, e2r_wh, e2r_wt,
-                                                        w1b, w2b, wcb);
-
-  k_relhist<<<NBR_, 256, 0, stream>>>(rel, Hrel);
-  k_relscan<<<1, 256, 0, stream>>>(Hrel, off_rel);
-  k_relscatter<<<NBR_, 256, 0, stream>>>(rel, hi, ti, Hrel, hr, tr);
-
-  k_count3<<<gTOT, TB, 0, stream>>>(ia, hi, ti, cnt_dest, cnt_h, cnt_t);
+  const int PTOT = 2*EH_*KP_ + 200*KP_ + N_*80;
+
+  k_pack_all<<<(PTOT + TB - 1)/TB, TB, 0, stream>>>(hw1_w, hw2_w, e2r_wh, e2r_wt,
+                                                    (const float4*)x_e,
+                                                    w1b, w2b, wcb, xbA);
+
+  k_build1<<<NBR_ + gTOT, TB, 0, stream>>>(rel, ia, hi, ti, Hrel, cnt_dest, cnt_h, cnt_t);
   k_scanA<<<3*NSB_, 256, 0, stream>>>(cnt_dest, cnt_h, cnt_t, bsum);
-  k_scanB<<<1, 64, 0, stream>>>(bsum, off_dest, off_h, off_t);
+  k_mid<<<2, 256, 0, stream>>>(Hrel, off_rel, bsum, off_dest, off_h, off_t);
   k_scanC<<<3*NSB_, 256, 0, stream>>>(cnt_dest, cnt_h, cnt_t, bsum,
                                       off_dest, off_h, off_t, dis);
-  k_scatter3<<<gTOT, TB, 0, stream>>>(ja, ia, rel, hi, ti,
-                                      off_dest, off_h, off_t,
-                                      cur_dest, cur_h, cur_t,
-                                      dis, j_dest, wj, relh, relt);
-
-  k_pack_x<<<gPKX, TB, 0, stream>>>((const float4*)x_e, EH4, xbA);
+  k_build2<<<NBR_ + gTOT, TB, 0, stream>>>(rel, hi, ti, Hrel, hr, tr,
+                                           ja, ia, off_dest, off_h, off_t,
+                                           cur_dest, cur_h, cur_t,
+                                           dis, j_dest, wj, relh, relt);
+
   gemm_mfma(xbA, w1b, g, EH_, N_, EH_, stream);
   k_gcn5<<<N_, 64, 0, stream>>>(off_dest, j_dest, wj, dis, xbA,
-                                (const float4*)x_e, EH4, (const float4*)g, hw1_b,
-                                (float4*)out, xbB);
+                                (const float4*)g, hw1_b, (float4*)out, xbB);
   gemm_mfma(xbB, w2b, g, EH_, N_, EH_, stream);
   k_gcn5<<<N_, 64, 0, stream>>>(off_dest, j_dest, wj, dis, xbB,
-                                (const float4*)out, LD4, (const float4*)g, hw2_b,
-                                (float4*)out, xbA);
+                                (const float4*)g, hw2_b, (float4*)out, xbA);
 
   gemm_mfma(xbA, wcb, xhxt, 200, N_, 200, stream);
   k_pproj<<<gN, TB, 0, stream>>>(xhxt, e2r_ah, e2r_at, (float4*)pht);
@@ -844,13 +885,10 @@
                                                (const float4*)xhxt, (float4*)xr_part);
   k_e2r_red2<<<R_, 64, 0, stream>>>((const float4*)xr_part, (float4*)xr, r2e_ar, sr8);
 
-  k_dots16b<<<(N_+15)/16, 256, 0, stream>>>(xbA, XBS_, EH_, 0, EH_, r2e_ah, r2e_at, st16, N_, 0);
-  k_fold_ht2<<<(N_+1)/2, 256, 0, stream>>>(off_h, off_t, relh, relt, st16, sr8, shp, stp);
-  k_r2e_agg2b<<<N_, 128, 0, stream>>>(off_h, off_t, relh, relt, shp, stp,
+  k_dots16b<<<(N_+15)/16, 256, 0, stream>>>(xbA, XBS_, EH_, EH_, r2e_ah, r2e_at, st16, N_);
+  k_r2e_fused<<<N_, 128, 0, stream>>>(off_h, off_t, relh, relt, st16, sr8,
                                       (const float4*)xr, (float4*)out, xeb);
 
-  k_dots16b<<<(N_+15)/16, 256, 0, stream>>>(xbA, XBS_, EH_, 0, 500, gat_ai, gat_aj, gg16, N_, 0);
-  k_dots16b<<<(N_+15)/16, 256, 0, stream>>>(xeb, XEBS_, 200, EH_, 500, gat_ai, gat_aj, gg16, N_, 1);
-  k_fold_gat2<<<(N_+3)/4, 256, 0, stream>>>(off_dest, j_dest, gg16, agp);
-  k_gat_agg4<<<N_, 128, 0, stream>>>(off_dest, j_dest, agp, xbA, xeb, (float4*)out);
-}
+  k_dots16g<<<(N_+15)/16, 256, 0, stream>>>(xbA, xeb, gat_ai, gat_aj, gg16, N_);
+  k_gat_fused<<<N_, 128, 0, stream>>>(off_dest, j_dest, gg16, xbA, xeb, (float4*)out);
+}
```
